# Kernel optimization log

Measured on AMD Instinct MI355X. Metric: run time of the kernel, lower is better.

## Reference

```python
import jax, jax.numpy as jnp
import numpy as np

CONF_THRESH = 0.01
TOP_K = 200
NMS_THRESH = 0.45


def setup_inputs() -> dict:
    key = jax.random.key(0)
    k1, k2, k3, k4, k5 = jax.random.split(key, 5)
    B, N, C = 32, 8732, 21
    return {
        "loc_data": jax.random.normal(k1, (B, N, 4), jnp.float32),
        "conf_data": jax.random.normal(k2, (B, N, C), jnp.float32),
        "pose_data": jax.random.normal(k3, (B, N, 32), jnp.float32),
        "line_data": jax.random.normal(k4, (B, N, 3), jnp.float32),
        "dbox_list": jax.random.uniform(k5, (N, 4), jnp.float32),
    }


def decode(loc, dbox):
    # loc, dbox: [N,4]; variances 0.1 / 0.2 as in the torch decode()
    cxcy = dbox[:, :2] + loc[:, :2] * 0.1 * dbox[:, 2:]
    wh = dbox[:, 2:] * jnp.exp(loc[:, 2:] * 0.2)
    mins = cxcy - wh / 2.0
    maxs = mins + wh
    return jnp.concatenate([mins, maxs], axis=1)  # [N,4] xyxy


def nms_class(boxes, scores, poses, lines):
    """Greedy NMS for one (batch, class). boxes [N,4], scores [N] (softmax probs).
    Matches torch nm_suppression: candidates are the top_k by score above
    conf_thresh; suppress IoU > overlap; at most top_k kept."""
    s0 = jnp.where(scores > CONF_THRESH, scores, -jnp.inf)
    _, cand_idx = jax.lax.top_k(s0, TOP_K)  # descending-score candidate pool
    cb = boxes[cand_idx]                     # [K,4]
    cs = s0[cand_idx]                        # [K], -inf where below threshold
    x1, y1, x2, y2 = cb[:, 0], cb[:, 1], cb[:, 2], cb[:, 3]
    area = (x2 - x1) * (y2 - y1)
    K = TOP_K
    ar = jnp.arange(K)

    def step(s, _):
        i = jnp.argmax(s)
        take = jnp.isfinite(s[i])
        xx1 = jnp.maximum(x1, x1[i])
        yy1 = jnp.maximum(y1, y1[i])
        xx2 = jnp.minimum(x2, x2[i])
        yy2 = jnp.minimum(y2, y2[i])
        inter = jnp.clip(xx2 - xx1, 0.0) * jnp.clip(yy2 - yy1, 0.0)
        union = area - inter + area[i]
        iou = inter / union
        supp = (iou > NMS_THRESH) | (ar == i)
        s_new = jnp.where(take & supp, -jnp.inf, s)
        return s_new, (i, take)

    _, (pos, take) = jax.lax.scan(step, cs, None, length=K)
    gi = cand_idx[pos]  # global box indices of kept detections [K]
    row = jnp.concatenate(
        [scores[gi][:, None], boxes[gi], poses[gi], lines[gi]], axis=1
    )  # [K, 1+4+32+3] = [200, 40]
    return row * take[:, None].astype(row.dtype)


def reference(loc_data, conf_data, pose_data, line_data, dbox_list):
    conf = jax.nn.softmax(conf_data, axis=-1)                       # [B,N,C]
    boxes = jax.vmap(decode, in_axes=(0, None))(loc_data, dbox_list)  # [B,N,4]
    per_cls = jax.vmap(nms_class, in_axes=(None, 1, None, None))    # over classes
    per_batch = jax.vmap(per_cls, in_axes=(0, 0, 0, 0))             # over batch
    out = per_batch(boxes, conf, pose_data, line_data)              # [B,C,200,40]
    return out.at[:, 0].set(0.0)  # class 0 (background) is skipped in torch loop
```

## Files before the change

kernel.cpp:

```cpp
#include <hip/hip_runtime.h>
#include <math.h>

#define BB 32
#define NN 8732
#define CC 21
#define TOPK 200
#define NPOSE 32
#define NLINE 3
#define NBINS 2048
#define CAP 1024
#define ROWW 40

__device__ __forceinline__ double fexp(double x) {
  const double LOG2E = 1.4426950408889634074;
  const double LN2HI = 6.93147180369123816490e-01;
  const double LN2LO = 1.90821492927058770002e-10;
  double kd = rint(x * LOG2E);
  double r = fma(-kd, LN2HI, x);
  r = fma(-kd, LN2LO, r);
  double p = 2.08767569878680989792e-09;
  p = fma(p, r, 2.50521083854417187751e-08);
  p = fma(p, r, 2.75573192239858906526e-07);
  p = fma(p, r, 2.75573192239858925110e-06);
  p = fma(p, r, 2.48015873015873015873e-05);
  p = fma(p, r, 1.98412698412698412698e-04);
  p = fma(p, r, 1.38888888888888888889e-03);
  p = fma(p, r, 8.33333333333333333333e-03);
  p = fma(p, r, 4.16666666666666666667e-02);
  p = fma(p, r, 1.66666666666666666667e-01);
  p = fma(p, r, 0.5);
  p = fma(p, r, 1.0);
  p = fma(p, r, 1.0);
  return ldexp(p, (int)kd);
}

__device__ __forceinline__ void softmax_es(const float* __restrict__ p, float* e,
                                           float& sumOut) {
  float m = p[0];
#pragma unroll
  for (int c = 1; c < CC; ++c) m = fmaxf(m, p[c]);
#pragma unroll
  for (int c = 0; c < CC; ++c) e[c] = (float)fexp((double)(p[c] - m));
  float r0 = e[0] + e[8], r1 = e[1] + e[9], r2 = e[2] + e[10], r3 = e[3] + e[11];
  float r4 = e[4] + e[12], r5 = e[5] + e[13], r6 = e[6] + e[14], r7 = e[7] + e[15];
  float res = ((r0 + r1) + (r2 + r3)) + ((r4 + r5) + (r6 + r7));
  res += e[16]; res += e[17]; res += e[18]; res += e[19]; res += e[20];
  sumOut = res;
}

__global__ __launch_bounds__(256) void score_kernel(
    const float* __restrict__ conf, float* __restrict__ scores) {
  __shared__ float buf[256 * CC];
  const int tid = threadIdx.x;
  const int i0 = blockIdx.x * 256;
  const int base = i0 * CC;
  int total = BB * NN * CC - base;
  if (total > 256 * CC) total = 256 * CC;
  for (int t = tid; t < total; t += 256) buf[t] = conf[base + t];
  __syncthreads();
  const int i = i0 + tid;
  if (i >= BB * NN) return;
  const float* p = buf + tid * CC;
  float e[CC], sum;
  softmax_es(p, e, sum);
  const int b = i / NN, n = i - b * NN;
#pragma unroll
  for (int c = 0; c < CC; ++c)
    scores[((size_t)b * CC + c) * NN + n] = e[c] / sum;
}

__global__ __launch_bounds__(256) void aux_kernel(
    const float* __restrict__ conf, float2* __restrict__ aux) {
  int i = blockIdx.x * 256 + threadIdx.x;
  if (i >= BB * NN) return;
  const float* p = conf + (size_t)i * CC;
  float e[CC], sum;
  softmax_es(p, e, sum);
  float m = p[0];
#pragma unroll
  for (int c = 1; c < CC; ++c) m = fmaxf(m, p[c]);
  aux[i] = make_float2(m, sum);
}

__global__ __launch_bounds__(256) void nms_kernel(
    const float* __restrict__ loc, const float* __restrict__ conf,
    const float* __restrict__ pose, const float* __restrict__ line,
    const float* __restrict__ dbox, const float* __restrict__ scores,
    const float2* __restrict__ aux, int mode, float* __restrict__ out) {
  const int bc = blockIdx.x;
  const int b = bc / CC, c = bc - b * CC;
  const int tid = threadIdx.x;
  float* outSlab = out + (size_t)bc * (TOPK * ROWW);

  {
    float4 z = make_float4(0.f, 0.f, 0.f, 0.f);
    float4* o4 = (float4*)outSlab;
    for (int i = tid; i < TOPK * ROWW / 4; i += 256) o4[i] = z;
  }
  if (c == 0) return;

  __shared__ int hist[NBINS];
  __shared__ int chunkSum[256];
  __shared__ float cscore[CAP];
  __shared__ int cidx[CAP];
  __shared__ float bx1[TOPK], by1[TOPK], bx2[TOPK], by2[TOPK], barea[TOPK];
  __shared__ int kept[TOPK];
  __shared__ int sBT, sCnt, sKept;

  for (int i = tid; i < NBINS; i += 256) hist[i] = 0;
  if (tid == 0) sCnt = 0;
  __syncthreads();

  const float* scoresB = scores + ((size_t)b * CC + c) * NN;
  const float2* auxB = aux + (size_t)b * NN;
  const float* confB = conf + (size_t)b * NN * CC + c;

  for (int n = tid; n < NN; n += 256) {
    float s;
    if (mode == 2) {
      s = scoresB[n];
    } else if (mode == 1) {
      float2 a = auxB[n];
      s = (float)fexp((double)(confB[(size_t)n * CC] - a.x)) / a.y;
    } else {
      const float* p = conf + ((size_t)b * NN + n) * CC;
      float e[CC], sum;
      softmax_es(p, e, sum);
      s = e[c] / sum;
    }
    if (s > 0.01f) {
      unsigned u = __float_as_uint(s);
      int bin = (int)(u >> 15) - 30720;
      bin = bin < 0 ? 0 : (bin > NBINS - 1 ? NBINS - 1 : bin);
      atomicAdd(&hist[bin], 1);
    }
  }
  __syncthreads();

  {
    int s8 = 0;
#pragma unroll
    for (int k = 0; k < 8; ++k) s8 += hist[tid * 8 + k];
    chunkSum[tid] = s8;
  }
  __syncthreads();
  if (tid == 0) {
    int cum = 0, bt = 0;
    for (int ch = 255; ch >= 0; --ch) {
      if (cum + chunkSum[ch] >= TOPK) {
        for (int bin = ch * 8 + 7;; --bin) {
          cum += hist[bin];
          if (cum >= TOPK || bin == ch * 8) { bt = bin; break; }
        }
        break;
      }
      cum += chunkSum[ch];
    }
    sBT = bt;
  }
  __syncthreads();
  const int bt = sBT;

  for (int n = tid; n < NN; n += 256) {
    float s;
    if (mode == 2) {
      s = scoresB[n];
    } else if (mode == 1) {
      float2 a = auxB[n];
      s = (float)fexp((double)(confB[(size_t)n * CC] - a.x)) / a.y;
    } else {
      const float* p = conf + ((size_t)b * NN + n) * CC;
      float e[CC], sum;
      softmax_es(p, e, sum);
      s = e[c] / sum;
    }
    if (s > 0.01f) {
      unsigned u = __float_as_uint(s);
      int bin = (int)(u >> 15) - 30720;
      bin = bin < 0 ? 0 : (bin > NBINS - 1 ? NBINS - 1 : bin);
      if (bin >= bt) {
        int p = atomicAdd(&sCnt, 1);
        if (p < CAP) { cscore[p] = s; cidx[p] = n; }
      }
    }
  }
  __syncthreads();
  const int M = sCnt < CAP ? sCnt : CAP;
  if (M == 0) return;

  int P = 1;
  while (P < M) P <<= 1;
  for (int i = M + tid; i < P; i += 256) {
    cscore[i] = -1e30f;
    cidx[i] = 0x7fffffff;
  }
  __syncthreads();
  for (int k = 2; k <= P; k <<= 1) {
    for (int j = k >> 1; j > 0; j >>= 1) {
      for (int i = tid; i < P; i += 256) {
        int ixj = i ^ j;
        if (ixj > i) {
          float si = cscore[i], sj = cscore[ixj];
          int ii = cidx[i], ij = cidx[ixj];
          bool agt = (si > sj) || (si == sj && ii < ij);
          bool up = ((i & k) == 0);
          if (up ? !agt : agt) {
            cscore[i] = sj; cscore[ixj] = si;
            cidx[i] = ij;  cidx[ixj] = ii;
          }
        }
      }
      __syncthreads();
    }
  }

  const int K = M < TOPK ? M : TOPK;

  const float* locB = loc + (size_t)b * NN * 4;
  for (int t = tid; t < K; t += 256) {
    int n = cidx[t];
    float l0 = locB[(size_t)n * 4 + 0], l1 = locB[(size_t)n * 4 + 1];
    float l2 = locB[(size_t)n * 4 + 2], l3 = locB[(size_t)n * 4 + 3];
    float d0 = dbox[(size_t)n * 4 + 0], d1 = dbox[(size_t)n * 4 + 1];
    float d2 = dbox[(size_t)n * 4 + 2], d3 = dbox[(size_t)n * 4 + 3];
    float cx = d0 + (l0 * 0.1f) * d2;
    float cy = d1 + (l1 * 0.1f) * d3;
    float w = d2 * (float)fexp((double)(l2 * 0.2f));
    float h = d3 * (float)fexp((double)(l3 * 0.2f));
    float x1 = cx - w * 0.5f;
    float y1 = cy - h * 0.5f;
    float x2 = x1 + w;
    float y2 = y1 + h;
    bx1[t] = x1; by1[t] = y1; bx2[t] = x2; by2[t] = y2;
    barea[t] = (x2 - x1) * (y2 - y1);
  }
  __syncthreads();

  if (tid < 64) {
    const int lane = tid;
    float X1[4], Y1[4], X2[4], Y2[4], AR[4];
    unsigned aliveBits = 0;
#pragma unroll
    for (int s = 0; s < 4; ++s) {
      int l = s * 64 + lane;
      if (l < K) {
        X1[s] = bx1[l]; Y1[s] = by1[l]; X2[s] = bx2[l]; Y2[s] = by2[l];
        AR[s] = barea[l];
        aliveBits |= 1u << s;
      } else {
        X1[s] = 0.f; Y1[s] = 0.f; X2[s] = 0.f; Y2[s] = 0.f; AR[s] = 0.f;
      }
    }
#pragma unroll
    for (int s = 0; s < 4; ++s) {
      int jmax = K - s * 64;
      if (jmax > 64) jmax = 64;
      for (int jj = 0; jj < jmax; ++jj) {
        unsigned abits = (unsigned)__shfl((int)aliveBits, jj, 64);
        if (!((abits >> s) & 1)) continue;
        const int j = s * 64 + jj;
        float x1j = __shfl(X1[s], jj, 64);
        float y1j = __shfl(Y1[s], jj, 64);
        float x2j = __shfl(X2[s], jj, 64);
        float y2j = __shfl(Y2[s], jj, 64);
        float aj  = __shfl(AR[s], jj, 64);
#pragma unroll
        for (int t2 = 0; t2 < 4; ++t2) {
          int l = t2 * 64 + lane;
          if (((aliveBits >> t2) & 1) && l > j) {
            float xx1 = fmaxf(X1[t2], x1j);
            float yy1 = fmaxf(Y1[t2], y1j);
            float xx2 = fminf(X2[t2], x2j);
            float yy2 = fminf(Y2[t2], y2j);
            float iw = fmaxf(xx2 - xx1, 0.0f);
            float ih = fmaxf(yy2 - yy1, 0.0f);
            float inter = iw * ih;
            float uni = (AR[t2] - inter) + aj;
            if (inter / uni > 0.45f) aliveBits &= ~(1u << t2);
          }
        }
      }
    }
    int base2 = 0;
#pragma unroll
    for (int s = 0; s < 4; ++s) {
      unsigned long long mb = __ballot((int)((aliveBits >> s) & 1));
      if ((aliveBits >> s) & 1) {
        int rank = base2 + __popcll(mb & ((1ull << lane) - 1));
        kept[rank] = s * 64 + lane;
      }
      base2 += __popcll(mb);
    }
    if (lane == 0) sKept = base2;
  }
  __syncthreads();

  const int nk = sKept;
  const float* poseB = pose + (size_t)b * NN * NPOSE;
  const float* lineB = line + (size_t)b * NN * NLINE;
  for (int t = tid; t < nk; t += 256) {
    int j = kept[t];
    int n = cidx[j];
    float* row = outSlab + (size_t)t * ROWW;
    row[0] = cscore[j];
    row[1] = bx1[j];
    row[2] = by1[j];
    row[3] = bx2[j];
    row[4] = by2[j];
#pragma unroll
    for (int q = 0; q < NPOSE; ++q) row[5 + q] = poseB[(size_t)n * NPOSE + q];
    row[37] = lineB[(size_t)n * NLINE + 0];
    row[38] = lineB[(size_t)n * NLINE + 1];
    row[39] = lineB[(size_t)n * NLINE + 2];
  }
}

extern "C" void kernel_launch(void* const* d_in, const int* in_sizes, int n_in,
                              void* d_out, int out_size, void* d_ws, size_t ws_size,
                              hipStream_t stream) {
  const float* loc  = (const float*)d_in[0];
  const float* conf = (const float*)d_in[1];
  const float* pose = (const float*)d_in[2];
  const float* line = (const float*)d_in[3];
  const float* dbox = (const float*)d_in[4];
  float* out = (float*)d_out;

  const size_t scoreBytes = (size_t)BB * CC * NN * sizeof(float);
  const size_t auxBytes   = (size_t)BB * NN * sizeof(float2);

  int mode;
  float* scores = nullptr;
  float2* aux = nullptr;
  if (ws_size >= scoreBytes) {
    mode = 2; scores = (float*)d_ws;
  } else if (ws_size >= auxBytes) {
    mode = 1; aux = (float2*)d_ws;
  } else {
    mode = 0;
  }

  const int total = BB * NN;
  if (mode == 2) {
    score_kernel<<<(total + 255) / 256, 256, 0, stream>>>(conf, scores);
  } else if (mode == 1) {
    aux_kernel<<<(total + 255) / 256, 256, 0, stream>>>(conf, aux);
  }
  nms_kernel<<<BB * CC, 256, 0, stream>>>(loc, conf, pose, line, dbox,
                                          scores, aux, mode, out);
}
```

Measured before the change: 204.3 us.

## Vectorize score loads, cache scores in registers across NMS passes, cheaper exp scaling

The mode-2 NMS path now loads each class's score row once into registers as float4 and reuses it for both the histogram and the candidate-collection passes, so the second global read goes away. The score kernel stages conf through shared memory with float4 loads and computes exp in place in shared memory with non-unrolled loops to cut register pressure. The fexp helper replaces ldexp with a clamped exponent bit-construction, and pose rows are gathered with float4 loads. The register-cached path hardcodes NN=8732 tiling (8×1024 + 135×4), and the in-place shared-memory exp may bring bank conflicts.

```diff
diff --git a/kernel.cpp b/kernel.cpp
--- a/kernel.cpp
+++ b/kernel.cpp
@@ -31,42 +31,43 @@
   p = fma(p, r, 0.5);
   p = fma(p, r, 1.0);
   p = fma(p, r, 1.0);
-  return ldexp(p, (int)kd);
-}
-
-__device__ __forceinline__ void softmax_es(const float* __restrict__ p, float* e,
-                                           float& sumOut) {
-  float m = p[0];
-#pragma unroll
-  for (int c = 1; c < CC; ++c) m = fmaxf(m, p[c]);
-#pragma unroll
-  for (int c = 0; c < CC; ++c) e[c] = (float)fexp((double)(p[c] - m));
-  float r0 = e[0] + e[8], r1 = e[1] + e[9], r2 = e[2] + e[10], r3 = e[3] + e[11];
-  float r4 = e[4] + e[12], r5 = e[5] + e[13], r6 = e[6] + e[14], r7 = e[7] + e[15];
-  float res = ((r0 + r1) + (r2 + r3)) + ((r4 + r5) + (r6 + r7));
-  res += e[16]; res += e[17]; res += e[18]; res += e[19]; res += e[20];
-  sumOut = res;
+  int k = (int)kd;
+  k = k < -1020 ? -1020 : (k > 1020 ? 1020 : k);
+  double sc = __longlong_as_double((long long)(1023 + k) << 52);
+  return p * sc;
 }
 
 __global__ __launch_bounds__(256) void score_kernel(
     const float* __restrict__ conf, float* __restrict__ scores) {
-  __shared__ float buf[256 * CC];
+  __shared__ __align__(16) float buf[256 * CC];
   const int tid = threadIdx.x;
   const int i0 = blockIdx.x * 256;
   const int base = i0 * CC;
   int total = BB * NN * CC - base;
   if (total > 256 * CC) total = 256 * CC;
-  for (int t = tid; t < total; t += 256) buf[t] = conf[base + t];
+  {
+    const float4* g4 = (const float4*)(conf + base);
+    float4* b4 = (float4*)buf;
+    const int n4 = total >> 2;
+    for (int t = tid; t < n4; t += 256) b4[t] = g4[t];
+  }
   __syncthreads();
   const int i = i0 + tid;
   if (i >= BB * NN) return;
-  const float* p = buf + tid * CC;
-  float e[CC], sum;
-  softmax_es(p, e, sum);
+  float* p = buf + tid * CC;
+  float m = p[0];
+#pragma unroll
+  for (int c = 1; c < CC; ++c) m = fmaxf(m, p[c]);
+#pragma unroll 1
+  for (int c = 0; c < CC; ++c) p[c] = (float)fexp((double)(p[c] - m));
+  float r0 = p[0] + p[8], r1 = p[1] + p[9], r2 = p[2] + p[10], r3 = p[3] + p[11];
+  float r4 = p[4] + p[12], r5 = p[5] + p[13], r6 = p[6] + p[14], r7 = p[7] + p[15];
+  float sum = ((r0 + r1) + (r2 + r3)) + ((r4 + r5) + (r6 + r7));
+  sum += p[16]; sum += p[17]; sum += p[18]; sum += p[19]; sum += p[20];
   const int b = i / NN, n = i - b * NN;
-#pragma unroll
+#pragma unroll 1
   for (int c = 0; c < CC; ++c)
-    scores[((size_t)b * CC + c) * NN + n] = e[c] / sum;
+    scores[((size_t)b * CC + c) * NN + n] = p[c] / sum;
 }
 
 __global__ __launch_bounds__(256) void aux_kernel(
@@ -74,12 +75,23 @@
   int i = blockIdx.x * 256 + threadIdx.x;
   if (i >= BB * NN) return;
   const float* p = conf + (size_t)i * CC;
-  float e[CC], sum;
-  softmax_es(p, e, sum);
   float m = p[0];
 #pragma unroll
   for (int c = 1; c < CC; ++c) m = fmaxf(m, p[c]);
+  float e[CC];
+#pragma unroll 1
+  for (int c = 0; c < CC; ++c) e[c] = (float)fexp((double)(p[c] - m));
+  float r0 = e[0] + e[8], r1 = e[1] + e[9], r2 = e[2] + e[10], r3 = e[3] + e[11];
+  float r4 = e[4] + e[12], r5 = e[5] + e[13], r6 = e[6] + e[14], r7 = e[7] + e[15];
+  float sum = ((r0 + r1) + (r2 + r3)) + ((r4 + r5) + (r6 + r7));
+  sum += e[16]; sum += e[17]; sum += e[18]; sum += e[19]; sum += e[20];
   aux[i] = make_float2(m, sum);
+}
+
+__device__ __forceinline__ int score_bin(float s) {
+  unsigned u = __float_as_uint(s);
+  int bin = (int)(u >> 15) - 30720;
+  return bin < 0 ? 0 : (bin > NBINS - 1 ? NBINS - 1 : bin);
 }
 
 __global__ __launch_bounds__(256) void nms_kernel(
@@ -115,70 +127,124 @@
   const float2* auxB = aux + (size_t)b * NN;
   const float* confB = conf + (size_t)b * NN * CC + c;
 
-  for (int n = tid; n < NN; n += 256) {
-    float s;
-    if (mode == 2) {
-      s = scoresB[n];
-    } else if (mode == 1) {
-      float2 a = auxB[n];
-      s = (float)fexp((double)(confB[(size_t)n * CC] - a.x)) / a.y;
-    } else {
-      const float* p = conf + ((size_t)b * NN + n) * CC;
-      float e[CC], sum;
-      softmax_es(p, e, sum);
-      s = e[c] / sum;
-    }
-    if (s > 0.01f) {
-      unsigned u = __float_as_uint(s);
-      int bin = (int)(u >> 15) - 30720;
-      bin = bin < 0 ? 0 : (bin > NBINS - 1 ? NBINS - 1 : bin);
-      atomicAdd(&hist[bin], 1);
-    }
-  }
-  __syncthreads();
-
-  {
-    int s8 = 0;
-#pragma unroll
-    for (int k = 0; k < 8; ++k) s8 += hist[tid * 8 + k];
-    chunkSum[tid] = s8;
-  }
-  __syncthreads();
-  if (tid == 0) {
-    int cum = 0, bt = 0;
-    for (int ch = 255; ch >= 0; --ch) {
-      if (cum + chunkSum[ch] >= TOPK) {
-        for (int bin = ch * 8 + 7;; --bin) {
-          cum += hist[bin];
-          if (cum >= TOPK || bin == ch * 8) { bt = bin; break; }
+  if (mode == 2) {
+    float4 v[9];
+#pragma unroll
+    for (int k = 0; k < 8; ++k)
+      v[k] = *(const float4*)(scoresB + k * 1024 + tid * 4);
+    if (tid < 135)
+      v[8] = *(const float4*)(scoresB + 8192 + tid * 4);
+    else
+      v[8] = make_float4(-1.f, -1.f, -1.f, -1.f);
+
+#pragma unroll
+    for (int k = 0; k < 9; ++k) {
+      float s0 = v[k].x, s1 = v[k].y, s2 = v[k].z, s3 = v[k].w;
+      if (s0 > 0.01f) atomicAdd(&hist[score_bin(s0)], 1);
+      if (s1 > 0.01f) atomicAdd(&hist[score_bin(s1)], 1);
+      if (s2 > 0.01f) atomicAdd(&hist[score_bin(s2)], 1);
+      if (s3 > 0.01f) atomicAdd(&hist[score_bin(s3)], 1);
+    }
+    __syncthreads();
+
+    {
+      int s8 = 0;
+#pragma unroll
+      for (int k = 0; k < 8; ++k) s8 += hist[tid * 8 + k];
+      chunkSum[tid] = s8;
+    }
+    __syncthreads();
+    if (tid == 0) {
+      int cum = 0, bt = 0;
+      for (int ch = 255; ch >= 0; --ch) {
+        if (cum + chunkSum[ch] >= TOPK) {
+          for (int bin = ch * 8 + 7;; --bin) {
+            cum += hist[bin];
+            if (cum >= TOPK || bin == ch * 8) { bt = bin; break; }
+          }
+          break;
         }
-        break;
-      }
-      cum += chunkSum[ch];
-    }
-    sBT = bt;
-  }
-  __syncthreads();
-  const int bt = sBT;
-
-  for (int n = tid; n < NN; n += 256) {
-    float s;
-    if (mode == 2) {
-      s = scoresB[n];
-    } else if (mode == 1) {
-      float2 a = auxB[n];
-      s = (float)fexp((double)(confB[(size_t)n * CC] - a.x)) / a.y;
-    } else {
-      const float* p = conf + ((size_t)b * NN + n) * CC;
-      float e[CC], sum;
-      softmax_es(p, e, sum);
-      s = e[c] / sum;
-    }
-    if (s > 0.01f) {
-      unsigned u = __float_as_uint(s);
-      int bin = (int)(u >> 15) - 30720;
-      bin = bin < 0 ? 0 : (bin > NBINS - 1 ? NBINS - 1 : bin);
-      if (bin >= bt) {
+        cum += chunkSum[ch];
+      }
+      sBT = bt;
+    }
+    __syncthreads();
+    const int bt = sBT;
+
+#pragma unroll
+    for (int k = 0; k < 9; ++k) {
+      float sv[4] = {v[k].x, v[k].y, v[k].z, v[k].w};
+#pragma unroll
+      for (int j = 0; j < 4; ++j) {
+        float s = sv[j];
+        if (s > 0.01f && score_bin(s) >= bt) {
+          int p = atomicAdd(&sCnt, 1);
+          if (p < CAP) { cscore[p] = s; cidx[p] = k * 1024 + tid * 4 + j; }
+        }
+      }
+    }
+  } else {
+    for (int n = tid; n < NN; n += 256) {
+      float s;
+      if (mode == 1) {
+        float2 a = auxB[n];
+        s = (float)fexp((double)(confB[(size_t)n * CC] - a.x)) / a.y;
+      } else {
+        const float* p = conf + ((size_t)b * NN + n) * CC;
+        float mm = p[0];
+        for (int c2 = 1; c2 < CC; ++c2) mm = fmaxf(mm, p[c2]);
+        float e[CC];
+        for (int c2 = 0; c2 < CC; ++c2) e[c2] = (float)fexp((double)(p[c2] - mm));
+        float r0 = e[0] + e[8], r1 = e[1] + e[9], r2 = e[2] + e[10], r3 = e[3] + e[11];
+        float r4 = e[4] + e[12], r5 = e[5] + e[13], r6 = e[6] + e[14], r7 = e[7] + e[15];
+        float sum = ((r0 + r1) + (r2 + r3)) + ((r4 + r5) + (r6 + r7));
+        sum += e[16]; sum += e[17]; sum += e[18]; sum += e[19]; sum += e[20];
+        s = e[c] / sum;
+      }
+      if (s > 0.01f) atomicAdd(&hist[score_bin(s)], 1);
+    }
+    __syncthreads();
+    {
+      int s8 = 0;
+#pragma unroll
+      for (int k = 0; k < 8; ++k) s8 += hist[tid * 8 + k];
+      chunkSum[tid] = s8;
+    }
+    __syncthreads();
+    if (tid == 0) {
+      int cum = 0, bt = 0;
+      for (int ch = 255; ch >= 0; --ch) {
+        if (cum + chunkSum[ch] >= TOPK) {
+          for (int bin = ch * 8 + 7;; --bin) {
+            cum += hist[bin];
+            if (cum >= TOPK || bin == ch * 8) { bt = bin; break; }
+          }
+          break;
+        }
+        cum += chunkSum[ch];
+      }
+      sBT = bt;
+    }
+    __syncthreads();
+    const int bt = sBT;
+    for (int n = tid; n < NN; n += 256) {
+      float s;
+      if (mode == 1) {
+        float2 a = auxB[n];
+        s = (float)fexp((double)(confB[(size_t)n * CC] - a.x)) / a.y;
+      } else {
+        const float* p = conf + ((size_t)b * NN + n) * CC;
+        float mm = p[0];
+        for (int c2 = 1; c2 < CC; ++c2) mm = fmaxf(mm, p[c2]);
+        float e[CC];
+        for (int c2 = 0; c2 < CC; ++c2) e[c2] = (float)fexp((double)(p[c2] - mm));
+        float r0 = e[0] + e[8], r1 = e[1] + e[9], r2 = e[2] + e[10], r3 = e[3] + e[11];
+        float r4 = e[4] + e[12], r5 = e[5] + e[13], r6 = e[6] + e[14], r7 = e[7] + e[15];
+        float sum = ((r0 + r1) + (r2 + r3)) + ((r4 + r5) + (r6 + r7));
+        sum += e[16]; sum += e[17]; sum += e[18]; sum += e[19]; sum += e[20];
+        s = e[c] / sum;
+      }
+      if (s > 0.01f && score_bin(s) >= bt) {
         int p = atomicAdd(&sCnt, 1);
         if (p < CAP) { cscore[p] = s; cidx[p] = n; }
       }
@@ -307,8 +373,15 @@
     row[2] = by1[j];
     row[3] = bx2[j];
     row[4] = by2[j];
-#pragma unroll
-    for (int q = 0; q < NPOSE; ++q) row[5 + q] = poseB[(size_t)n * NPOSE + q];
+    const float4* p4 = (const float4*)(poseB + (size_t)n * NPOSE);
+#pragma unroll
+    for (int q = 0; q < 8; ++q) {
+      float4 pv = p4[q];
+      row[5 + 4 * q + 0] = pv.x;
+      row[5 + 4 * q + 1] = pv.y;
+      row[5 + 4 * q + 2] = pv.z;
+      row[5 + 4 * q + 3] = pv.w;
+    }
     row[37] = lineB[(size_t)n * NLINE + 0];
     row[38] = lineB[(size_t)n * NLINE + 1];
     row[39] = lineB[(size_t)n * NLINE + 2];
```

Measured after the change: 192.0 us. 6.0% less time.
